# Performance work log

Measured on AMD Instinct MI355X. Metric: run time of the kernel, lower is better.

The kernel has to match this reference:

```python
import jax, jax.numpy as jnp
import numpy as np

B, D, T = 16, 64, 8192
K = 1024          # num_embeddings
EPS = 1e-5
DECAY = 0.99


def setup_inputs() -> dict:
    key = jax.random.key(0)
    k1, k2 = jax.random.split(key)
    x = jax.random.normal(k1, (B, D, T), dtype=jnp.float32)
    # xavier_uniform over [K, D]
    limit = float(np.sqrt(6.0 / (K + D)))
    embeddings = jax.random.uniform(k2, (K, D), dtype=jnp.float32, minval=-limit, maxval=limit)
    return {"x": x, "embeddings": embeddings}


def reference(x, embeddings):
    """Training-mode forward of VectorQuantizerEMA1D, first EMA step.

    With hidden=0 and counter incremented to 1, the bias-corrected EMA
    average equals the raw value: avg = value*(1-decay)/(1-decay**1) = value.
    Returns (quantized [B,D,T], updated embeddings [K,D]).
    """
    num_embeddings, embedding_dim = embeddings.shape
    xt = jnp.transpose(x, (0, 2, 1))                 # [B, T, D]
    flat_x = xt.reshape(-1, embedding_dim)           # [N, D]

    # squared-euclidean distances [N, K]
    distances = (
        jnp.sum(flat_x ** 2, axis=1, keepdims=True)
        + jnp.sum(embeddings ** 2, axis=1)
        - 2.0 * flat_x @ embeddings.T
    )
    idx = jnp.argmin(distances, axis=1)              # [N]

    quantized = embeddings[idx].reshape(xt.shape)    # [B, T, D]

    # EMA codebook update (first step -> average == value)
    counts = jax.ops.segment_sum(
        jnp.ones_like(idx, dtype=flat_x.dtype), idx, num_segments=num_embeddings)
    n = jnp.sum(counts)
    cluster_size = (counts + EPS) / (n + num_embeddings * EPS) * n
    dw = jax.ops.segment_sum(flat_x, idx, num_segments=num_embeddings)  # [K, D]
    new_embeddings = dw / cluster_size[:, None]

    # straight-through estimator
    quantized_st = xt + jax.lax.stop_gradient(quantized - xt)
    out = jnp.transpose(quantized_st, (0, 2, 1))     # [B, D, T]
    return out, new_embeddings
```

## Files before the change

### kernel.cpp

```cpp
#include <hip/hip_runtime.h>

#define K_CODES 1024
#define DIM 64
#define B_ 16
#define T_ 8192
#define N_ (B_*T_)
#define EPSF 1e-5f
#define SMARGIN 5e-4f
#define MSK7 0xFFFFFF80u

typedef __attribute__((ext_vector_type(8))) short short8;
typedef __attribute__((ext_vector_type(4))) float f32x4;

typedef __attribute__((address_space(1))) unsigned char g1_t;
typedef __attribute__((address_space(3))) unsigned char l3_t;

__device__ __forceinline__ unsigned bf16_rne(float f) {
    unsigned u = __float_as_uint(f);
    return (u + 0x7fffu + ((u >> 16) & 1u)) >> 16;
}
__device__ __forceinline__ unsigned umx(unsigned a, unsigned b) { return a > b ? a : b; }
__device__ __forceinline__ unsigned umn(unsigned a, unsigned b) { return a < b ? a : b; }

__global__ __launch_bounds__(64) void vq_prep(const float* __restrict__ emb,
                                              double* __restrict__ e64,
                                              double* __restrict__ snh64,
                                              float* __restrict__ snb32,
                                              unsigned short* __restrict__ ehib,
                                              unsigned short* __restrict__ elob,
                                              int* __restrict__ counts,
                                              int* __restrict__ cnt2,
                                              int* __restrict__ flagcnt) {
    const int k = blockIdx.x;
    const int d = threadIdx.x;
    if (d == 0) counts[k] = 0;
    if (d == 1) cnt2[k] = 0;
    if (k == 0 && d == 2) *flagcnt = 0;

    const float ef = emb[k * DIM + d];
    const unsigned rh = bf16_rne(ef);
    const float hif = __uint_as_float(rh << 16);
    const float lof = ef - hif;
    const unsigned rl = bf16_rne(lof);
    ehib[k * DIM + d] = (unsigned short)rh;
    elob[k * DIM + d] = (unsigned short)rl;

    const double ed = (double)ef;
    e64[k * DIM + d] = ed;
    double s = ed * ed;
    #pragma unroll
    for (int off = 32; off; off >>= 1) s += __shfl_down(s, off, 64);
    if (d == 0) {
        snh64[k] = 0.5 * s;
        snb32[k] = (float)(16.0 - 0.5 * s);
    }
}

__global__ __launch_bounds__(256) void vq_screen(const float* __restrict__ x,
                                                 const unsigned short* __restrict__ ehib,
                                                 const unsigned short* __restrict__ elob,
                                                 const float* __restrict__ snb32,
                                                 const float* __restrict__ emb,
                                                 float* __restrict__ out,
                                                 float* __restrict__ xT,
                                                 int* __restrict__ idx32,
                                                 int* __restrict__ counts,
                                                 int* __restrict__ flagcnt,
                                                 int* __restrict__ flagids,
                                                 int use_xt) {
    __shared__ unsigned short stg[2][2][2048];
    __shared__ float red[128][4];
    __shared__ int sidx[128];
    __shared__ int hcnt[K_CODES];

    const int tid   = threadIdx.x;
    const int wid   = tid >> 6;
    const int lane  = tid & 63;
    const int vgrp  = wid & 1;
    const int khalf = wid >> 1;
    const int ln15  = lane & 15;
    const int lhi   = lane >> 4;

    #pragma unroll
    for (int q = 0; q < 4; q++) hcnt[tid + q * 256] = 0;

    const int blk  = blockIdx.x;
    const int b    = blk >> 6;
    const int tblk = (blk & 63) << 7;
    const int t0   = tblk + vgrp * 64;
    const float* xb = x + ((size_t)b << 19);

    short8 xbh[4][2], xbl[4][2];
    #pragma unroll
    for (int nt = 0; nt < 4; nt++) {
        const int t = t0 + nt * 16 + ln15;
        #pragma unroll
        for (int s = 0; s < 2; s++) {
            #pragma unroll
            for (int j = 0; j < 8; j++) {
                const int d = s * 32 + lhi * 8 + j;
                const float xf = xb[((size_t)d << 13) + t];
                const unsigned rh = bf16_rne(xf);
                const float hif = __uint_as_float(rh << 16);
                const unsigned rl = bf16_rne(xf - hif);
                xbh[nt][s][j] = (short)rh;
                xbl[nt][s][j] = (short)rl;
            }
        }
    }

    const int srow = lane >> 3;
    const int soff = (srow << 7) + (((lane & 7) ^ srow) << 4);
    const int rx = ln15 & 7;
    const int c0 = (lhi ^ rx) << 3;
    const int c1 = ((4 + lhi) ^ rx) << 3;
    const int rbase = ln15 * 64;

    const int kbase = khalf << 9;

#define STAGE(BUF, KT) { \
    const size_t tb_ = (size_t)(kbase + ((KT) << 4)) * DIM; \
    if (vgrp == 0) { \
        const unsigned char* g_ = (const unsigned char*)(ehib + tb_) + soff; \
        unsigned short* l_ = &stg[khalf][BUF][0]; \
        __builtin_amdgcn_global_load_lds((const g1_t*)g_,          (l3_t*)l_,          16, 0, 0); \
        __builtin_amdgcn_global_load_lds((const g1_t*)(g_ + 1024), (l3_t*)(l_ + 512),  16, 0, 0); \
    } else { \
        const unsigned char* g_ = (const unsigned char*)(elob + tb_) + soff; \
        unsigned short* l_ = &stg[khalf][BUF][1024]; \
        __builtin_amdgcn_global_load_lds((const g1_t*)g_,          (l3_t*)l_,          16, 0, 0); \
        __builtin_amdgcn_global_load_lds((const g1_t*)(g_ + 1024), (l3_t*)(l_ + 512),  16, 0, 0); \
    } \
}

    unsigned b1k[4] = {0, 0, 0, 0}, b2k[4] = {0, 0, 0, 0};

#define BODY(BUF, KT, DOPRE, NKT) { \
    if (DOPRE) STAGE((BUF) ^ 1, NKT) \
    const unsigned short* lb = &stg[khalf][BUF][0]; \
    const short8 ah0 = *(const short8*)(lb + rbase + c0); \
    const short8 ah1 = *(const short8*)(lb + rbase + c1); \
    const short8 al0 = *(const short8*)(lb + 1024 + rbase + c0); \
    const short8 al1 = *(const short8*)(lb + 1024 + rbase + c1); \
    const int k0_ = kbase + ((KT) << 4); \
    const f32x4 bias = *(const f32x4*)(snb32 + k0_ + lhi * 4); \
    const unsigned revb = 127u - (unsigned)((KT) << 2); \
    _Pragma("unroll") \
    for (int nt = 0; nt < 4; nt++) { \
        f32x4 acc = bias; \
        acc = __builtin_amdgcn_mfma_f32_16x16x32_bf16(ah0, xbh[nt][0], acc, 0, 0, 0); \
        acc = __builtin_amdgcn_mfma_f32_16x16x32_bf16(ah1, xbh[nt][1], acc, 0, 0, 0); \
        acc = __builtin_amdgcn_mfma_f32_16x16x32_bf16(ah0, xbl[nt][0], acc, 0, 0, 0); \
        acc = __builtin_amdgcn_mfma_f32_16x16x32_bf16(ah1, xbl[nt][1], acc, 0, 0, 0); \
        acc = __builtin_amdgcn_mfma_f32_16x16x32_bf16(al0, xbh[nt][0], acc, 0, 0, 0); \
        acc = __builtin_amdgcn_mfma_f32_16x16x32_bf16(al1, xbh[nt][1], acc, 0, 0, 0); \
        _Pragma("unroll") \
        for (int r = 0; r < 4; r++) { \
            const unsigned key = (__float_as_uint(acc[r]) & MSK7) | (revb - r); \
            b2k[nt] = umx(b2k[nt], umn(b1k[nt], key)); \
            b1k[nt] = umx(b1k[nt], key); \
        } \
    } \
    __syncthreads(); \
}

    STAGE(0, 0)
    __syncthreads();
    #pragma unroll 1
    for (int kt2 = 0; kt2 < 32; kt2 += 2) {
        BODY(0, kt2, 1, kt2 + 1)
        BODY(1, kt2 + 1, (kt2 < 30), kt2 + 2)
    }
#undef STAGE
#undef BODY

    #pragma unroll
    for (int nt = 0; nt < 4; nt++) {
        float B1 = __uint_as_float(b1k[nt] & MSK7);
        float B2 = __uint_as_float(b2k[nt] & MSK7);
        const int local = 127 - (int)(b1k[nt] & 127u);
        int I = kbase + ((local >> 2) << 4) + lhi * 4 + (local & 3);
        #pragma unroll
        for (int off = 16; off <= 32; off <<= 1) {
            const float o1 = __shfl_xor(B1, off, 64);
            const float o2 = __shfl_xor(B2, off, 64);
            const int   oi = __shfl_xor(I,  off, 64);
            const float nb2 = fmaxf(fminf(B1, o1), fmaxf(B2, o2));
            if (o1 > B1 || (o1 == B1 && oi < I)) { B1 = o1; I = oi; }
            B2 = nb2;
        }
        if (khalf == 1 && lane < 16) {
            const int vloc = vgrp * 64 + nt * 16 + lane;
            red[vloc][0] = B1; red[vloc][1] = B2; red[vloc][2] = __int_as_float(I);
        }
        b1k[nt] = __float_as_uint(B1); b2k[nt] = __float_as_uint(B2);
        if (lane < 16 && khalf == 0) sidx[vgrp * 64 + nt * 16 + lane] = I;
    }
    __syncthreads();

    if (khalf == 0) {
        #pragma unroll
        for (int nt = 0; nt < 4; nt++) {
            if (lane < 16) {
                const int vloc = vgrp * 64 + nt * 16 + lane;
                const float ob1 = red[vloc][0];
                const float ob2 = red[vloc][1];
                const int   oi  = __float_as_int(red[vloc][2]);
                float B1 = __uint_as_float(b1k[nt]);
                float B2 = __uint_as_float(b2k[nt]);
                int I = sidx[vloc];
                if (ob1 > B1) { B2 = fmaxf(B1, ob2); B1 = ob1; I = oi; }
                else          { B2 = fmaxf(B2, ob1); }
                sidx[vloc] = (B1 - B2 <= SMARGIN) ? -1 : I;
            }
        }
    }
    __syncthreads();

    const int vloc = tid & 127;
    const int dh   = tid >> 7;
    const int t    = tblk + vloc;
    const int I    = sidx[vloc];
    const int v    = (b << 13) + t;

    float xf[32];
    #pragma unroll
    for (int j = 0; j < 32; j++) xf[j] = xb[((size_t)(dh * 32 + j) << 13) + t];

    if (use_xt) {
        float4* xtp = (float4*)(xT + (size_t)v * 64 + dh * 32);
        #pragma unroll
        for (int q = 0; q < 8; q++) {
            float4 w; w.x = xf[q*4]; w.y = xf[q*4+1]; w.z = xf[q*4+2]; w.w = xf[q*4+3];
            xtp[q] = w;
        }
    }

    if (I < 0) {
        if (dh == 0) { const int p = atomicAdd(flagcnt, 1); flagids[p] = v; }
    } else {
        if (dh == 0) { idx32[v] = I; atomicAdd(&hcnt[I], 1); }
        const float4* eq4 = (const float4*)(emb + I * DIM + dh * 32);
        #pragma unroll
        for (int q = 0; q < 8; q++) {
            const float4 e4 = eq4[q];
            const int d = dh * 32 + q * 4;
            out[((size_t)b << 19) + ((size_t)(d + 0) << 13) + t] = xf[q*4+0] + (e4.x - xf[q*4+0]);
            out[((size_t)b << 19) + ((size_t)(d + 1) << 13) + t] = xf[q*4+1] + (e4.y - xf[q*4+1]);
            out[((size_t)b << 19) + ((size_t)(d + 2) << 13) + t] = xf[q*4+2] + (e4.z - xf[q*4+2]);
            out[((size_t)b << 19) + ((size_t)(d + 3) << 13) + t] = xf[q*4+3] + (e4.w - xf[q*4+3]);
        }
    }
    __syncthreads();
    #pragma unroll
    for (int q = 0; q < 4; q++) {
        const int c = hcnt[tid + q * 256];
        if (c) atomicAdd(&counts[tid + q * 256], c);
    }
}

__global__ __launch_bounds__(256) void vq_rescan(const float* __restrict__ x,
                                                 const float* __restrict__ emb,
                                                 const double* __restrict__ e64,
                                                 const double* __restrict__ snh64,
                                                 float* __restrict__ out,
                                                 int* __restrict__ idx32,
                                                 int* __restrict__ counts,
                                                 const int* __restrict__ flagcnt,
                                                 const int* __restrict__ flagids) {
    __shared__ double rb[4][4];
    __shared__ int    ri[4][4];
    __shared__ int    rf[4];
    const int tid   = threadIdx.x;
    const int wid   = tid >> 6;
    const int lane  = tid & 63;
    const int cslot = lane >> 2;
    const int dg    = lane & 3;
    const int count = *flagcnt;

    for (int base = blockIdx.x * 4; base < count; base += gridDim.x * 4) {
        bool act[4]; int vv[4];
        const float* xbp[4];
        double xd[4][16];
        #pragma unroll
        for (int vx = 0; vx < 4; vx++) {
            const int i = base + vx;
            act[vx] = i < count;
            const int v = flagids[act[vx] ? i : 0];
            vv[vx] = v;
            const int b = v >> 13, t = v & (T_ - 1);
            xbp[vx] = x + ((size_t)b << 19) + t;
            #pragma unroll
            for (int j = 0; j < 16; j++)
                xd[vx][j] = act[vx] ? (double)xbp[vx][(size_t)(dg * 16 + j) << 13] : 0.0;
        }

        double best[4] = {-1e300, -1e300, -1e300, -1e300};
        int    bi_[4]  = {0, 0, 0, 0};
        const int kq = wid << 8;

        #pragma unroll 4
        for (int cc = 0; cc < 16; cc++) {
            const int k = kq + cc * 16 + cslot;
            const double* ek = e64 + (size_t)k * DIM + dg * 16;
            const double snh = snh64[k];
            #pragma unroll
            for (int vx = 0; vx < 4; vx++) {
                double a0 = 0.0, a1 = 0.0, a2 = 0.0, a3 = 0.0;
                #pragma unroll
                for (int j = 0; j < 16; j += 4) {
                    a0 = __fma_rn(xd[vx][j + 0], ek[j + 0], a0);
                    a1 = __fma_rn(xd[vx][j + 1], ek[j + 1], a1);
                    a2 = __fma_rn(xd[vx][j + 2], ek[j + 2], a2);
                    a3 = __fma_rn(xd[vx][j + 3], ek[j + 3], a3);
                }
                double a = (a0 + a1) + (a2 + a3);
                a += __shfl_xor(a, 1, 64);
                a += __shfl_xor(a, 2, 64);
                const double m = a - snh;
                if (m > best[vx]) { best[vx] = m; bi_[vx] = k; }
            }
        }

        #pragma unroll
        for (int vx = 0; vx < 4; vx++) {
            double bb = best[vx]; int ii = bi_[vx];
            #pragma unroll
            for (int off = 4; off <= 32; off <<= 1) {
                const double ob = __shfl_xor(bb, off, 64);
                const int    oi = __shfl_xor(ii, off, 64);
                if (ob > bb || (ob == bb && oi < ii)) { bb = ob; ii = oi; }
            }
            if (lane == 0) { rb[wid][vx] = bb; ri[wid][vx] = ii; }
        }
        __syncthreads();
        if (tid < 4) {
            double bb = rb[0][tid]; int ii = ri[0][tid];
            #pragma unroll
            for (int w = 1; w < 4; w++) {
                if (rb[w][tid] > bb) { bb = rb[w][tid]; ii = ri[w][tid]; }
            }
            rf[tid] = ii;
        }
        __syncthreads();

        {
            const int vx = wid;
            if (act[vx]) {
                const int v = vv[vx];
                const int b = v >> 13, t = v & (T_ - 1);
                const int I = rf[vx];
                const float xf = xbp[vx][(size_t)lane << 13];
                out[((size_t)b << 19) + ((size_t)lane << 13) + t] =
                    xf + (emb[I * DIM + lane] - xf);
                if (lane == 0) { idx32[v] = I; atomicAdd(&counts[I], 1); }
            }
        }
        __syncthreads();
    }
}

__global__ __launch_bounds__(1024) void vq_scatter(const int* __restrict__ idx32,
                                                   const int* __restrict__ counts,
                                                   int* __restrict__ cnt2,
                                                   int* __restrict__ offsets,
                                                   int* __restrict__ order) {
    __shared__ int soff[K_CODES];
    __shared__ int wtot[16];
    const int tid  = threadIdx.x;
    const int lane = tid & 63;
    const int w    = tid >> 6;

    const int c = counts[tid];
    int s = c;
    #pragma unroll
    for (int off = 1; off < 64; off <<= 1) {
        const int o = __shfl_up(s, off, 64);
        if (lane >= off) s += o;
    }
    if (lane == 63) wtot[w] = s;
    __syncthreads();
    if (tid < 16) {
        int ws_ = wtot[tid];
        #pragma unroll
        for (int off = 1; off < 16; off <<= 1) {
            const int o = __shfl_up(ws_, off, 64);
            if (tid >= off) ws_ += o;
        }
        wtot[tid] = ws_;
    }
    __syncthreads();
    const int wbase = (w > 0) ? wtot[w - 1] : 0;
    soff[tid] = wbase + s - c;
    __syncthreads();
    if (blockIdx.x == 0) offsets[tid] = soff[tid];

    const int v = blockIdx.x * 1024 + tid;
    const int k = idx32[v];
    const int p = soff[k] + atomicAdd(&cnt2[k], 1);
    order[p] = v;
}

__global__ __launch_bounds__(256) void vq_reduce8(const float* __restrict__ xT,
                                                  const int* __restrict__ order,
                                                  const int* __restrict__ offsets,
                                                  const int* __restrict__ counts,
                                                  float* __restrict__ partials) {
    __shared__ int lv[1024];
    __shared__ float ps[4][64];
    const int k   = blockIdx.x >> 3;
    const int sl  = blockIdx.x & 7;
    const int tid = threadIdx.x;
    const int i4  = tid >> 6;
    const int d   = tid & 63;
    const int cnt = counts[k];
    const int chunk = (cnt + 7) >> 3;
    const int lo = sl * chunk;
    const int hi = min(cnt, lo + chunk);
    const int off = offsets[k] + lo;
    const int n = hi - lo;

    float sum = 0.f;
    for (int base = 0; base < n; base += 1024) {
        const int m = min(1024, n - base);
        __syncthreads();
        for (int i = tid; i < m; i += 256) lv[i] = order[off + base + i];
        __syncthreads();
        float s0 = 0.f, s1 = 0.f, s2 = 0.f, s3 = 0.f;
        int i = i4;
        for (; i + 12 < m; i += 16) {
            s0 += xT[(size_t)lv[i] * 64 + d];
            s1 += xT[(size_t)lv[i + 4] * 64 + d];
            s2 += xT[(size_t)lv[i + 8] * 64 + d];
            s3 += xT[(size_t)lv[i + 12] * 64 + d];
        }
        for (; i < m; i += 4) s0 += xT[(size_t)lv[i] * 64 + d];
        sum += (s0 + s1) + (s2 + s3);
    }
    __syncthreads();
    ps[i4][d] = sum;
    __syncthreads();
    if (i4 == 0)
        partials[(((size_t)sl << 10) + k) * 64 + d] = ps[0][d] + ps[1][d] + ps[2][d] + ps[3][d];
}

__global__ __launch_bounds__(64) void vq_fin(const float* __restrict__ partials,
                                             const int* __restrict__ counts,
                                             float* __restrict__ newemb) {
    const int k = blockIdx.x;
    const int d = threadIdx.x;
    float tot = 0.f;
    #pragma unroll
    for (int sl = 0; sl < 8; sl++) tot += partials[(((size_t)sl << 10) + k) * 64 + d];
    const float c = (float)counts[k];
    const float cluster = (c + EPSF) / (131072.0f + 1024.0f * EPSF) * 131072.0f;
    newemb[k * DIM + d] = tot / cluster;
}

__global__ __launch_bounds__(256) void vq_reduce(const float* __restrict__ x,
                                                 const float* __restrict__ xT,
                                                 const int* __restrict__ order,
                                                 const int* __restrict__ offsets,
                                                 const int* __restrict__ counts,
                                                 float* __restrict__ newemb,
                                                 int use_xt) {
    __shared__ int lv[1024];
    __shared__ float ps[4][64];
    const int k = blockIdx.x;
    const int tid = threadIdx.x;
    const int i4 = tid >> 6;
    const int d = tid & 63;
    const int off = offsets[k];
    const int cnt = counts[k];
    float sum = 0.f;
    for (int base = 0; base < cnt; base += 1024) {
        const int m = min(1024, cnt - base);
        __syncthreads();
        for (int i = tid; i < m; i += 256) lv[i] = order[off + base + i];
        __syncthreads();
        if (use_xt) {
            for (int i = i4; i < m; i += 4) sum += xT[(size_t)lv[i] * 64 + d];
        } else {
            for (int i = i4; i < m; i += 4) {
                const int v = lv[i];
                sum += x[((size_t)(v >> 13) << 19) + ((size_t)d << 13) + (v & (T_ - 1))];
            }
        }
    }
    __syncthreads();
    ps[i4][d] = sum;
    __syncthreads();
    if (i4 == 0) {
        const float tot = ps[0][d] + ps[1][d] + ps[2][d] + ps[3][d];
        const float c = (float)cnt;
        const float cluster = (c + EPSF) / (131072.0f + 1024.0f * EPSF) * 131072.0f;
        newemb[k * DIM + d] = tot / cluster;
    }
}

extern "C" void kernel_launch(void* const* d_in, const int* in_sizes, int n_in,
                              void* d_out, int out_size, void* d_ws, size_t ws_size,
                              hipStream_t stream) {
    const float* x   = (const float*)d_in[0];
    const float* emb = (const float*)d_in[1];

    char* ws = (char*)d_ws;
    double*         e64     = (double*)(ws);
    double*         snh64   = (double*)(ws + 524288);
    float*          snb32   = (float*)(ws + 532480);
    unsigned short* ehib    = (unsigned short*)(ws + 536576);
    unsigned short* elob    = (unsigned short*)(ws + 667648);
    int*            idx32   = (int*)(ws + 798720);
    int*            order   = (int*)(ws + 1323008);
    int*            counts  = (int*)(ws + 1847296);
    int*            flagcnt = (int*)(ws + 1851392);
    int*            offsets = (int*)(ws + 1851456);
    int*            cnt2    = (int*)(ws + 1855552);
    int*            flagids = (int*)(ws + 1859648);
    float*          xT      = (float*)(ws + 2383936);
    float*          part8   = (float*)(ws + 35938368);
    const int use_xt = (ws_size >= (size_t)2383936 + 33554432) ? 1 : 0;
    const int use_p8 = (use_xt && ws_size >= (size_t)35938368 + 2097152) ? 1 : 0;

    float* out    = (float*)d_out;
    float* newemb = out + (size_t)B_ * DIM * T_;

    vq_prep<<<K_CODES, 64, 0, stream>>>(emb, e64, snh64, snb32, ehib, elob,
                                        counts, cnt2, flagcnt);
    vq_screen<<<N_ / 128, 256, 0, stream>>>(x, ehib, elob, snb32, emb, out, xT, idx32,
                                            counts, flagcnt, flagids, use_xt);
    vq_rescan<<<2048, 256, 0, stream>>>(x, emb, e64, snh64, out, idx32, counts,
                                        flagcnt, flagids);
    vq_scatter<<<N_ / 1024, 1024, 0, stream>>>(idx32, counts, cnt2, offsets, order);
    if (use_p8) {
        vq_reduce8<<<K_CODES * 8, 256, 0, stream>>>(xT, order, offsets, counts, part8);
        vq_fin<<<K_CODES, 64, 0, stream>>>(part8, counts, newemb);
    } else {
        vq_reduce<<<K_CODES, 256, 0, stream>>>(x, xT, order, offsets, counts, newemb, use_xt);
    }
}
```

Measured before the change: 168.7 us.

## Triple-buffer codebook staging with single barrier and cache bias in LDS

Moves the codebook tile pipeline in the screening kernel from double to triple buffering. Each step now does an explicit vmcnt wait plus one s_barrier before prefetching two tiles ahead, instead of a trailing __syncthreads after every tile. The per-code bias vector is loaded once into LDS asynchronously rather than read from global memory each step. The MFMA section also runs at raised wave priority. LDS use grows by about 12 KB per block, which may lower occupancy, and the hand-counted vmcnt values must stay in step with the number of loads issued.

```diff
diff --git a/kernel.cpp b/kernel.cpp
--- a/kernel.cpp
+++ b/kernel.cpp
@@ -68,7 +68,8 @@
                                                  int* __restrict__ flagcnt,
                                                  int* __restrict__ flagids,
                                                  int use_xt) {
-    __shared__ unsigned short stg[2][2][2048];
+    __shared__ unsigned short stg[2][3][2048];
+    __shared__ float snl[K_CODES];
     __shared__ float red[128][4];
     __shared__ int sidx[128];
     __shared__ int hcnt[K_CODES];
@@ -89,6 +90,13 @@
     const int tblk = (blk & 63) << 7;
     const int t0   = tblk + vgrp * 64;
     const float* xb = x + ((size_t)b << 19);
+
+    if (vgrp == 0) {
+        const unsigned char* gs = (const unsigned char*)(snb32 + (khalf << 9));
+        unsigned char* ls = (unsigned char*)&snl[khalf << 9];
+        __builtin_amdgcn_global_load_lds((const g1_t*)(gs + lane * 16),        (l3_t*)ls,          16, 0, 0);
+        __builtin_amdgcn_global_load_lds((const g1_t*)(gs + 1024 + lane * 16), (l3_t*)(ls + 1024), 16, 0, 0);
+    }
 
     short8 xbh[4][2], xbl[4][2];
     #pragma unroll
@@ -135,16 +143,19 @@
 
     unsigned b1k[4] = {0, 0, 0, 0}, b2k[4] = {0, 0, 0, 0};
 
-#define BODY(BUF, KT, DOPRE, NKT) { \
-    if (DOPRE) STAGE((BUF) ^ 1, NKT) \
-    const unsigned short* lb = &stg[khalf][BUF][0]; \
+#define BODY(CBUF, KT, DOPRE, NBUF, VM) { \
+    asm volatile("s_waitcnt vmcnt(" VM ")" ::: "memory");    \
+    asm volatile("s_barrier" ::: "memory");                  \
+    if (DOPRE) STAGE(NBUF, (KT) + 2) \
+    const unsigned short* lb = &stg[khalf][CBUF][0]; \
     const short8 ah0 = *(const short8*)(lb + rbase + c0); \
     const short8 ah1 = *(const short8*)(lb + rbase + c1); \
     const short8 al0 = *(const short8*)(lb + 1024 + rbase + c0); \
     const short8 al1 = *(const short8*)(lb + 1024 + rbase + c1); \
     const int k0_ = kbase + ((KT) << 4); \
-    const f32x4 bias = *(const f32x4*)(snb32 + k0_ + lhi * 4); \
+    const f32x4 bias = *(const f32x4*)(&snl[k0_ + lhi * 4]); \
     const unsigned revb = 127u - (unsigned)((KT) << 2); \
+    __builtin_amdgcn_s_setprio(1); \
     _Pragma("unroll") \
     for (int nt = 0; nt < 4; nt++) { \
         f32x4 acc = bias; \
@@ -161,16 +172,19 @@
             b1k[nt] = umx(b1k[nt], key); \
         } \
     } \
-    __syncthreads(); \
+    __builtin_amdgcn_s_setprio(0); \
 }
 
     STAGE(0, 0)
-    __syncthreads();
+    STAGE(1, 1)
     #pragma unroll 1
-    for (int kt2 = 0; kt2 < 32; kt2 += 2) {
-        BODY(0, kt2, 1, kt2 + 1)
-        BODY(1, kt2 + 1, (kt2 < 30), kt2 + 2)
-    }
+    for (int kt3 = 0; kt3 < 30; kt3 += 3) {
+        BODY(0, kt3,     1, 2, "2")
+        BODY(1, kt3 + 1, 1, 0, "2")
+        BODY(2, kt3 + 2, 1, 1, "2")
+    }
+    BODY(0, 30, 0, 0, "2")
+    BODY(1, 31, 0, 0, "0")
 #undef STAGE
 #undef BODY
 
```

Result: faster. 163.7 us (-3.0%).
